# Kernel optimization log

Measured on AMD Instinct MI355X. Metric: run time of the kernel, lower is better.

The kernel has to match this reference:

```python
import jax, jax.numpy as jnp
import numpy as np

EMBED_DIM = 768
NUM_HEADS = 12
HEAD_DIM = EMBED_DIM // NUM_HEADS
B, N = 4, 2048


def setup_inputs() -> dict:
    key = jax.random.key(0)
    k_x, k_wqkv, k_bqkv, k_wo, k_bo = jax.random.split(key, 5)
    s = 1.0 / np.sqrt(EMBED_DIM)
    return {
        "x": jax.random.normal(k_x, (B, N, EMBED_DIM), dtype=jnp.float32),
        # torch nn.Linear weight layout: [out_features, in_features]
        "w_qkv": jax.random.uniform(k_wqkv, (3 * EMBED_DIM, EMBED_DIM), minval=-s, maxval=s, dtype=jnp.float32),
        "b_qkv": jax.random.uniform(k_bqkv, (3 * EMBED_DIM,), minval=-s, maxval=s, dtype=jnp.float32),
        "w_out": jax.random.uniform(k_wo, (EMBED_DIM, EMBED_DIM), minval=-s, maxval=s, dtype=jnp.float32),
        "b_out": jax.random.uniform(k_bo, (EMBED_DIM,), minval=-s, maxval=s, dtype=jnp.float32),
    }


def reference(x, w_qkv, b_qkv, w_out, b_out):
    Bsz, Nlen, C = x.shape
    # fused QKV projection: [B, N, 3C]
    qkv = jnp.einsum("bnc,oc->bno", x, w_qkv) + b_qkv
    qkv = qkv.reshape(Bsz, Nlen, 3, NUM_HEADS, HEAD_DIM)
    q = qkv[:, :, 0].transpose(0, 2, 1, 3)  # [B, H, N, D]
    k = qkv[:, :, 1].transpose(0, 2, 1, 3)
    v = qkv[:, :, 2].transpose(0, 2, 1, 3)
    scale = 1.0 / np.sqrt(HEAD_DIM).astype(np.float32)
    scores = jnp.einsum("bhqd,bhkd->bhqk", q, k) * scale  # [B, H, N, N]
    attn = jax.nn.softmax(scores, axis=-1)
    ctx = jnp.einsum("bhqk,bhkd->bhqd", attn, v)  # [B, H, N, D]
    ctx = ctx.transpose(0, 2, 1, 3).reshape(Bsz, Nlen, C)
    return jnp.einsum("bnc,oc->bno", ctx, w_out) + b_out
```

## Files before the change

kernel.cpp:

```cpp
#include <hip/hip_runtime.h>
#include <math.h>

typedef __attribute__((ext_vector_type(8))) short bf16x8;
typedef __attribute__((ext_vector_type(4))) float f32x4;
typedef unsigned short u16;

namespace {
constexpr int BATCH = 4, SEQ = 2048, CDIM = 768, NH = 12, HD = 64;
constexpr int MROWS = BATCH * SEQ;
constexpr int KD = CDIM;
constexpr float QSCALE = 0.125f * 1.44269504088896f;
}

__device__ __forceinline__ u16 f2bf(float f) {
  unsigned x = __float_as_uint(f);
  return (u16)((x + 0x7fffu + ((x >> 16) & 1u)) >> 16);
}

__device__ __forceinline__ unsigned pk2bf(float a, float b) {
  unsigned r;
  asm("v_cvt_pk_bf16_f32 %0, %1, %2" : "=v"(r) : "v"(a), "v"(b));
  return r;
}

#if defined(__has_builtin)
#if __has_builtin(__builtin_amdgcn_exp2f)
#define EXP2(x) __builtin_amdgcn_exp2f(x)
#endif
#endif
#ifndef EXP2
#define EXP2(x) exp2f(x)
#endif

#define GLD16(gp, lp)                                                        \
  __builtin_amdgcn_global_load_lds(                                          \
      (const __attribute__((address_space(1))) void*)(gp),                   \
      (__attribute__((address_space(3))) void*)(lp), 16, 0, 0)

__global__ void convert_bf16(const float* __restrict__ x, u16* __restrict__ xb, int nx4,
                             const float* __restrict__ w1, u16* __restrict__ w1b, int n14,
                             const float* __restrict__ w2, u16* __restrict__ w2b, int n24) {
  const int stride = gridDim.x * blockDim.x;
  const int t0 = blockIdx.x * blockDim.x + threadIdx.x;
  for (int i = t0; i < nx4; i += stride) {
    float4 v = ((const float4*)x)[i];
    ushort4 o; o.x = f2bf(v.x); o.y = f2bf(v.y); o.z = f2bf(v.z); o.w = f2bf(v.w);
    ((ushort4*)xb)[i] = o;
  }
  for (int i = t0; i < n14; i += stride) {
    float4 v = ((const float4*)w1)[i];
    ushort4 o; o.x = f2bf(v.x); o.y = f2bf(v.y); o.z = f2bf(v.z); o.w = f2bf(v.w);
    ((ushort4*)w1b)[i] = o;
  }
  for (int i = t0; i < n24; i += stride) {
    float4 v = ((const float4*)w2)[i];
    ushort4 o; o.x = f2bf(v.x); o.y = f2bf(v.y); o.z = f2bf(v.z); o.w = f2bf(v.w);
    ((ushort4*)w2b)[i] = o;
  }
}

template <int MODE>
__global__ __launch_bounds__(256, 4) void gemm_bf16(
    const u16* __restrict__ A, const u16* __restrict__ Bw,
    const float* __restrict__ bias, float* __restrict__ outf,
    u16* __restrict__ qws, u16* __restrict__ kws, u16* __restrict__ vws) {
  __shared__ u16 smem[2 * 128 * 64];
  u16* As = smem;
  u16* Bs = smem + 128 * 64;
  const int t = threadIdx.x;
  const int w = t >> 6, l = t & 63, g = l >> 4, li = l & 15;
  const int wm = w >> 1, wn = w & 1;
  const int lin = blockIdx.x;
  const int rowb = ((lin & 7) << 3) | ((lin >> 3) & 7);
  const int colb = lin >> 6;
  const int row0 = rowb * 128, col0 = colb * 128;

  const int srow = w * 32 + (l >> 3);
  const int skc = (l & 7) ^ (l >> 3);
  const u16* gA = A + (size_t)(row0 + srow) * KD + skc * 8;
  const u16* gB = Bw + (size_t)(col0 + srow) * KD + skc * 8;

  f32x4 acc[4][4];
#pragma unroll
  for (int a = 0; a < 4; ++a)
#pragma unroll
    for (int c = 0; c < 4; ++c) acc[a][c] = {0.f, 0.f, 0.f, 0.f};

  for (int k0 = 0; k0 < KD; k0 += 64) {
    __syncthreads();
#pragma unroll
    for (int j = 0; j < 4; ++j) {
      GLD16(gA + (size_t)8 * j * KD + k0, &As[(w * 32 + 8 * j) * 64]);
      GLD16(gB + (size_t)8 * j * KD + k0, &Bs[(w * 32 + 8 * j) * 64]);
    }
    __syncthreads();

    bf16x8 af[4][2], bfr[4][2];
#pragma unroll
    for (int mi = 0; mi < 4; ++mi) {
      const int r = wm * 64 + mi * 16 + li;
#pragma unroll
      for (int ks = 0; ks < 2; ++ks)
        af[mi][ks] = *(const bf16x8*)&As[r * 64 + (((ks * 4 + g) ^ (li & 7)) * 8)];
    }
#pragma unroll
    for (int ni = 0; ni < 4; ++ni) {
      const int r = wn * 64 + ni * 16 + li;
#pragma unroll
      for (int ks = 0; ks < 2; ++ks)
        bfr[ni][ks] = *(const bf16x8*)&Bs[r * 64 + (((ks * 4 + g) ^ (li & 7)) * 8)];
    }
#pragma unroll
    for (int ni = 0; ni < 4; ++ni)
#pragma unroll
      for (int mi = 0; mi < 4; ++mi) {
        acc[mi][ni] = __builtin_amdgcn_mfma_f32_16x16x32_bf16(af[mi][0], bfr[ni][0], acc[mi][ni], 0, 0, 0);
        acc[mi][ni] = __builtin_amdgcn_mfma_f32_16x16x32_bf16(af[mi][1], bfr[ni][1], acc[mi][ni], 0, 0, 0);
      }
  }

  float bsr[4];
#pragma unroll
  for (int ni = 0; ni < 4; ++ni) bsr[ni] = bias[col0 + wn * 64 + ni * 16 + li];
  const int bidx = row0 >> 11;
  const int nseq0 = row0 & (SEQ - 1);

  __syncthreads();

  if (MODE == 1) {
    float* Cf = (float*)smem;
#pragma unroll
    for (int p = 0; p < 4; ++p) {
      if (wm == (p >> 1)) {
#pragma unroll
        for (int m2 = 0; m2 < 2; ++m2) {
          const int mi = (p & 1) * 2 + m2;
#pragma unroll
          for (int ni = 0; ni < 4; ++ni)
#pragma unroll
            for (int i = 0; i < 4; ++i)
              Cf[(m2 * 16 + 4 * g + i) * 132 + wn * 64 + ni * 16 + li] =
                  acc[mi][ni][i] + bsr[ni];
        }
      }
      __syncthreads();
#pragma unroll
      for (int j = 0; j < 4; ++j) {
        const int fid = t + 256 * j;
        const int r = fid >> 5, c4 = (fid & 31) * 4;
        *(float4*)(outf + (size_t)(row0 + p * 32 + r) * CDIM + col0 + c4) =
            *(const float4*)&Cf[r * 132 + c4];
      }
      __syncthreads();
    }
  } else {
#pragma unroll
    for (int hc = 0; hc < 2; ++hc) {
      const int nb = col0 + hc * 64;
      const int s = nb / CDIM;
      const int h = (nb % CDIM) / HD;
      if (wn == hc) {
        if (s < 2) {
          const float qs = (s == 0) ? QSCALE : 1.f;
#pragma unroll
          for (int mi = 0; mi < 4; ++mi)
#pragma unroll
            for (int ni = 0; ni < 4; ++ni)
#pragma unroll
              for (int i = 0; i < 4; ++i)
                smem[(wm * 64 + mi * 16 + 4 * g + i) * 72 + ni * 16 + li] =
                    f2bf((acc[mi][ni][i] + bsr[ni]) * qs);
        } else {
#pragma unroll
          for (int mi = 0; mi < 4; ++mi)
#pragma unroll
            for (int ni = 0; ni < 4; ++ni)
#pragma unroll
              for (int i = 0; i < 4; ++i)
                smem[(ni * 16 + li) * 136 + wm * 64 + mi * 16 + 4 * g + i] =
                    f2bf(acc[mi][ni][i] + bsr[ni]);
        }
      }
      __syncthreads();
      if (s < 2) {
        u16* dst = (s == 0 ? qws : kws) + ((size_t)(bidx * NH + h) * SEQ + nseq0) * HD;
        const int r = t >> 3, c = (t & 7) * 8;
#pragma unroll
        for (int rd = 0; rd < 4; ++rd)
          *(uint4*)(dst + (size_t)(r + 32 * rd) * HD + c) =
              *(const uint4*)&smem[(r + 32 * rd) * 72 + c];
      } else {
        u16* dst = vws + (size_t)(bidx * NH + h) * HD * SEQ + nseq0;
        const int d = t >> 4, c = (t & 15) * 8;
#pragma unroll
        for (int rd = 0; rd < 4; ++rd)
          *(uint4*)(dst + (size_t)(d + 16 * rd) * SEQ + c) =
              *(const uint4*)&smem[(d + 16 * rd) * 136 + c];
      }
      __syncthreads();
    }
  }
}

__global__ __launch_bounds__(256, 3) void attn_mfma(
    const u16* __restrict__ qws, const u16* __restrict__ kws,
    const u16* __restrict__ vws, u16* __restrict__ ctx) {
  __shared__ u16 Ks[2][64 * 64];
  __shared__ u16 Vs[2][64 * 64];
  __shared__ u16 Ps[4 * 32 * 72];
  const int t = threadIdx.x;
  const int w = t >> 6, l = t & 63, g = l >> 4, li = l & 15;
  const int q0 = blockIdx.x * 128;
  const int h = blockIdx.y, b = blockIdx.z;
  const size_t bh = (size_t)b * NH + h;
  const u16* qb = qws + bh * SEQ * HD;
  const u16* kb = kws + bh * SEQ * HD;
  const u16* vb = vws + bh * HD * SEQ;

  bf16x8 qf[2][2];
#pragma unroll
  for (int qt = 0; qt < 2; ++qt)
#pragma unroll
    for (int ks = 0; ks < 2; ++ks)
      qf[qt][ks] = *(const bf16x8*)(qb + (size_t)(q0 + w * 32 + qt * 16 + li) * HD + ks * 32 + g * 8);
  asm volatile("s_waitcnt vmcnt(0)" ::: "memory");
  __builtin_amdgcn_sched_barrier(0);

  f32x4 acc[4][2];
#pragma unroll
  for (int dt = 0; dt < 4; ++dt)
#pragma unroll
    for (int qt = 0; qt < 2; ++qt) acc[dt][qt] = {0.f, 0.f, 0.f, 0.f};
  float lrun[2] = {0.f, 0.f};

  const int srow8 = l >> 3;
  const int skc = (l & 7) ^ srow8;
  const u16* gK = kb + (size_t)(w * 16 + srow8) * HD + skc * 8;
  const u16* gV = vb + (size_t)(w * 16 + srow8) * SEQ + skc * 8;
  u16* Pw = Ps + w * 32 * 72;

  constexpr int NT = SEQ / 64;

#define STAGE(kt_, buf_)                                                          \
  do {                                                                            \
    const int key0_ = (kt_) * 64;                                                 \
    GLD16(gK + (size_t)(key0_ + 0) * HD, &Ks[buf_][(w * 16 + 0) * 64]);           \
    GLD16(gV + (size_t)0 * SEQ + key0_, &Vs[buf_][(w * 16 + 0) * 64]);            \
    GLD16(gK + (size_t)(key0_ + 8) * HD, &Ks[buf_][(w * 16 + 8) * 64]);           \
    GLD16(gV + (size_t)8 * SEQ + key0_, &Vs[buf_][(w * 16 + 8) * 64]);            \
  } while (0)

  STAGE(0, 0);
  STAGE(1, 1);

  const f32x4 Z = {0.f, 0.f, 0.f, 0.f};

  for (int kt = 0; kt < NT; ++kt) {
    const int cur = kt & 1;
    const u16* KsC = Ks[cur];
    const u16* VsC = Vs[cur];
    if (kt + 1 < NT) { asm volatile("s_waitcnt vmcnt(4)" ::: "memory"); }
    else             { asm volatile("s_waitcnt vmcnt(0)" ::: "memory"); }
    __builtin_amdgcn_sched_barrier(0);
    __builtin_amdgcn_s_barrier();
    __builtin_amdgcn_sched_barrier(0);

    f32x4 S[4][2];
    __builtin_amdgcn_s_setprio(1);
#pragma unroll
    for (int kb4 = 0; kb4 < 4; ++kb4) {
      bf16x8 kf0 = *(const bf16x8*)&KsC[(kb4 * 16 + li) * 64 + ((g ^ (li & 7)) * 8)];
      bf16x8 kf1 = *(const bf16x8*)&KsC[(kb4 * 16 + li) * 64 + (((4 + g) ^ (li & 7)) * 8)];
#pragma unroll
      for (int qt = 0; qt < 2; ++qt) {
        S[kb4][qt] = __builtin_amdgcn_mfma_f32_16x16x32_bf16(kf0, qf[qt][0], Z, 0, 0, 0);
        S[kb4][qt] = __builtin_amdgcn_mfma_f32_16x16x32_bf16(kf1, qf[qt][1], S[kb4][qt], 0, 0, 0);
      }
    }
    __builtin_amdgcn_s_setprio(0);

#pragma unroll
    for (int qt = 0; qt < 2; ++qt) {
      float rs = 0.f;
#pragma unroll
      for (int kb4 = 0; kb4 < 4; ++kb4) {
        const float p0 = EXP2(S[kb4][qt][0]);
        const float p1 = EXP2(S[kb4][qt][1]);
        const float p2 = EXP2(S[kb4][qt][2]);
        const float p3 = EXP2(S[kb4][qt][3]);
        rs += (p0 + p1) + (p2 + p3);
        uint2 pk;
        pk.x = pk2bf(p0, p1);
        pk.y = pk2bf(p2, p3);
        *(uint2*)&Pw[(qt * 16 + li) * 72 + ((kb4 ^ (li & 3)) * 16) + 4 * g] = pk;
      }
      rs += __shfl_xor(rs, 16);
      rs += __shfl_xor(rs, 32);
      lrun[qt] += rs;
    }

    bf16x8 vf[4][2];
#pragma unroll
    for (int dt = 0; dt < 4; ++dt) {
      vf[dt][0] = *(const bf16x8*)&VsC[(dt * 16 + li) * 64 + ((g ^ (li & 7)) * 8)];
      vf[dt][1] = *(const bf16x8*)&VsC[(dt * 16 + li) * 64 + (((4 + g) ^ (li & 7)) * 8)];
    }
    bf16x8 pf[2][2];
#pragma unroll
    for (int qt = 0; qt < 2; ++qt)
#pragma unroll
      for (int ks = 0; ks < 2; ++ks) {
        const int slot = (ks * 2 + (g >> 1)) ^ (li & 3);
        pf[qt][ks] = *(const bf16x8*)&Pw[(qt * 16 + li) * 72 + slot * 16 + (g & 1) * 8];
      }
    asm volatile("s_waitcnt lgkmcnt(0)" ::: "memory");
    __builtin_amdgcn_sched_barrier(0);
    __builtin_amdgcn_s_barrier();
    __builtin_amdgcn_sched_barrier(0);
    if (kt + 2 < NT) STAGE(kt + 2, cur);

    __builtin_amdgcn_s_setprio(1);
#pragma unroll
    for (int dt = 0; dt < 4; ++dt)
#pragma unroll
      for (int qt = 0; qt < 2; ++qt) {
        acc[dt][qt] = __builtin_amdgcn_mfma_f32_16x16x32_bf16(vf[dt][0], pf[qt][0], acc[dt][qt], 0, 0, 0);
        acc[dt][qt] = __builtin_amdgcn_mfma_f32_16x16x32_bf16(vf[dt][1], pf[qt][1], acc[dt][qt], 0, 0, 0);
      }
    __builtin_amdgcn_s_setprio(0);
  }
#undef STAGE

  float inv[2] = {1.f / lrun[0], 1.f / lrun[1]};
#pragma unroll
  for (int qt = 0; qt < 2; ++qt)
#pragma unroll
    for (int dt = 0; dt < 4; ++dt) {
      uint2 pk;
      pk.x = pk2bf(acc[dt][qt][0] * inv[qt], acc[dt][qt][1] * inv[qt]);
      pk.y = pk2bf(acc[dt][qt][2] * inv[qt], acc[dt][qt][3] * inv[qt]);
      *(uint2*)&Ps[(w * 32 + qt * 16 + li) * 72 + dt * 16 + 4 * g] = pk;
    }
  __syncthreads();
  {
    const int r = t >> 3, c = (t & 7) * 8;
#pragma unroll
    for (int rd = 0; rd < 4; ++rd)
      *(uint4*)(ctx + ((size_t)b * SEQ + q0 + r + 32 * rd) * CDIM + h * HD + c) =
          *(const uint4*)&Ps[(r + 32 * rd) * 72 + c];
  }
}

extern "C" void kernel_launch(void* const* d_in, const int* in_sizes, int n_in,
                              void* d_out, int out_size, void* d_ws, size_t ws_size,
                              hipStream_t stream) {
  (void)in_sizes; (void)n_in; (void)out_size; (void)ws_size;
  const float* x     = (const float*)d_in[0];
  const float* w_qkv = (const float*)d_in[1];
  const float* b_qkv = (const float*)d_in[2];
  const float* w_out = (const float*)d_in[3];
  const float* b_out = (const float*)d_in[4];
  float* out = (float*)d_out;

  u16* xb    = (u16*)d_ws;
  u16* wqkvb = xb + (size_t)MROWS * KD;
  u16* wob   = wqkvb + (size_t)3 * CDIM * KD;
  u16* qb    = wob + (size_t)CDIM * KD;
  const size_t QS = (size_t)BATCH * NH * SEQ * HD;
  u16* kb   = qb + QS;
  u16* vb   = kb + QS;
  u16* ctxb = vb + QS;

  hipLaunchKernelGGL(convert_bf16, dim3(2048), dim3(256), 0, stream,
                     x, xb, MROWS * KD / 4,
                     w_qkv, wqkvb, 3 * CDIM * KD / 4,
                     w_out, wob, CDIM * KD / 4);
  hipLaunchKernelGGL((gemm_bf16<0>), dim3((MROWS / 128) * (3 * CDIM / 128)), dim3(256), 0,
                     stream, xb, wqkvb, b_qkv, nullptr, qb, kb, vb);
  hipLaunchKernelGGL(attn_mfma, dim3(SEQ / 128, NH, BATCH), dim3(256), 0, stream,
                     qb, kb, vb, ctxb);
  hipLaunchKernelGGL((gemm_bf16<1>), dim3((MROWS / 128) * (CDIM / 128)), dim3(256), 0,
                     stream, ctxb, wob, b_out, out, nullptr, nullptr, nullptr);
}
```

Baseline: 203.1 us.

## Overlap next-tile global-to-LDS loads with MFMA compute in projection GEMM

Restructures the GEMM k-loop so that after fragments are read from LDS into registers, the next k-tile's global-to-LDS loads are issued before the MFMA block runs, letting memory latency hide behind compute. Explicit waitcnt, s_barrier and sched_barrier calls replace __syncthreads, and s_setprio raises wave priority around the MFMAs. It keeps a single LDS buffer, so correctness depends on the LDS reads finishing before the barrier, which the lgkmcnt(0) wait enforces. Manual barriers add fragility.

New measurement: 272.9 us. 1.34x slower.

```diff
diff --git a/kernel.cpp b/kernel.cpp
--- a/kernel.cpp
+++ b/kernel.cpp
@@ -86,15 +86,23 @@
 #pragma unroll
     for (int c = 0; c < 4; ++c) acc[a][c] = {0.f, 0.f, 0.f, 0.f};
 
-  for (int k0 = 0; k0 < KD; k0 += 64) {
-    __syncthreads();
-#pragma unroll
-    for (int j = 0; j < 4; ++j) {
-      GLD16(gA + (size_t)8 * j * KD + k0, &As[(w * 32 + 8 * j) * 64]);
-      GLD16(gB + (size_t)8 * j * KD + k0, &Bs[(w * 32 + 8 * j) * 64]);
-    }
-    __syncthreads();
-
+#define GSTAGE(k0_)                                                           \
+  do {                                                                        \
+    _Pragma("unroll")                                                         \
+    for (int j = 0; j < 4; ++j) {                                             \
+      GLD16(gA + (size_t)8 * j * KD + (k0_), &As[(w * 32 + 8 * j) * 64]);     \
+      GLD16(gB + (size_t)8 * j * KD + (k0_), &Bs[(w * 32 + 8 * j) * 64]);     \
+    }                                                                         \
+  } while (0)
+
+  constexpr int NK = KD / 64;
+  GSTAGE(0);
+  asm volatile("s_waitcnt vmcnt(0)" ::: "memory");
+  __builtin_amdgcn_sched_barrier(0);
+  __builtin_amdgcn_s_barrier();
+  __builtin_amdgcn_sched_barrier(0);
+
+  for (int kk = 0; kk < NK; ++kk) {
     bf16x8 af[4][2], bfr[4][2];
 #pragma unroll
     for (int mi = 0; mi < 4; ++mi) {
@@ -110,6 +118,14 @@
       for (int ks = 0; ks < 2; ++ks)
         bfr[ni][ks] = *(const bf16x8*)&Bs[r * 64 + (((ks * 4 + g) ^ (li & 7)) * 8)];
     }
+    asm volatile("s_waitcnt lgkmcnt(0)" ::: "memory");
+    __builtin_amdgcn_sched_barrier(0);
+    __builtin_amdgcn_s_barrier();
+    __builtin_amdgcn_sched_barrier(0);
+
+    if (kk + 1 < NK) GSTAGE((kk + 1) * 64);
+
+    __builtin_amdgcn_s_setprio(1);
 #pragma unroll
     for (int ni = 0; ni < 4; ++ni)
 #pragma unroll
@@ -117,7 +133,16 @@
         acc[mi][ni] = __builtin_amdgcn_mfma_f32_16x16x32_bf16(af[mi][0], bfr[ni][0], acc[mi][ni], 0, 0, 0);
         acc[mi][ni] = __builtin_amdgcn_mfma_f32_16x16x32_bf16(af[mi][1], bfr[ni][1], acc[mi][ni], 0, 0, 0);
       }
-  }
+    __builtin_amdgcn_s_setprio(0);
+
+    if (kk + 1 < NK) {
+      asm volatile("s_waitcnt vmcnt(0)" ::: "memory");
+      __builtin_amdgcn_sched_barrier(0);
+      __builtin_amdgcn_s_barrier();
+      __builtin_amdgcn_sched_barrier(0);
+    }
+  }
+#undef GSTAGE
 
   float bsr[4];
 #pragma unroll
```
